# Kernel tuning notes

Hardware: AMD Instinct MI355X
Metric: run time of the kernel (lower is better)

The kernel has to match this reference:

```python
import jax, jax.numpy as jnp
import numpy as np

N_HEADS, D_MODEL, D_KEY = 16, 1024, 64
B, T = 8, 512
SCALE = D_KEY ** (-0.5)


def setup_inputs() -> dict:
    key = jax.random.key(0)
    k1, k2, k3, k4, k5, k6 = jax.random.split(key, 6)
    return {
        "v": jax.random.normal(k1, (B, T, D_MODEL), jnp.float32),
        "mask": jax.random.randint(k2, (B, T, T), 0, 2).astype(bool),
        "w_kqs_w": 0.02 * jax.random.normal(k3, (2 * N_HEADS * D_KEY, D_MODEL), jnp.float32),
        "w_kqs_b": 0.02 * jax.random.normal(k4, (2 * N_HEADS * D_KEY,), jnp.float32),
        "fc_w": 0.02 * jax.random.normal(k5, (D_MODEL, N_HEADS * D_MODEL), jnp.float32),
        "fc_b": 0.02 * jax.random.normal(k6, (D_MODEL,), jnp.float32),
    }


def reference(v, mask, w_kqs_w, w_kqs_b, fc_w, fc_b):
    b, t, d = v.shape
    # kq projection: [b,t,2*H*dk] -> split as (head, 2*dk) per einops 'b t (head k)'
    kq = v @ w_kqs_w.T + w_kqs_b
    kq = kq.reshape(b, t, N_HEADS, 2 * D_KEY).transpose(2, 0, 1, 3)  # [h,b,t,2dk]
    k, q = jnp.split(kq, 2, axis=-1)  # each [h,b,t,dk]
    attn = jnp.einsum('hbqd,hbkd->hbqk', q, k) * SCALE  # [h,b,t,t]
    attn = jnp.where(mask, jnp.float32(-100000.0), attn)  # mask [b,t,t] broadcasts over heads
    attn = jax.nn.softmax(attn, axis=-1)
    # non-projected V broadcast across heads: out [h,b,t,d_model]
    out = jnp.einsum('hbqk,bkc->hbqc', attn, v)
    out = out.transpose(1, 2, 0, 3).reshape(b, t, N_HEADS * d)  # 'head b t c -> b t (head c)'
    out = out @ fc_w.T + fc_b
    return out, attn
```

## Files before the change

kernel.cpp:

```cpp
#include <hip/hip_runtime.h>
#include <cstdint>


typedef __attribute__((ext_vector_type(8))) short short8;
typedef __attribute__((ext_vector_type(4))) float f32x4;

__device__ __forceinline__ unsigned short f2bf(float x) {
  unsigned int u = __float_as_uint(x);
  u += 0x7FFFu + ((u >> 16) & 1u);
  return (unsigned short)(u >> 16);
}

__device__ __forceinline__ void gld16(void* lds, const void* g) {
  __builtin_amdgcn_global_load_lds(
      (const __attribute__((address_space(1))) void*)g,
      (__attribute__((address_space(3))) void*)lds, 16, 0, 0);
}

template<int N> __device__ __forceinline__ void wait_barrier() {
  if constexpr (N == 0)      asm volatile("s_waitcnt vmcnt(0)\n\ts_barrier" ::: "memory");
  else if constexpr (N == 3) asm volatile("s_waitcnt vmcnt(3)\n\ts_barrier" ::: "memory");
  else if constexpr (N == 4) asm volatile("s_waitcnt vmcnt(4)\n\ts_barrier" ::: "memory");
  else static_assert(N < 0, "unsupported vmcnt");
}

template<int BM>
__device__ __forceinline__ void gemm_bt(
    const short* __restrict__ A, int lda,
    const short* __restrict__ B, int ldb,
    int klen, short* __restrict__ ldsA, short* __restrict__ ldsB,
    f32x4 acc[4][4])
{
  constexpr int THREADS = 2 * BM;
  constexpr int NLOADS = (BM == 256) ? 3 : 4;
  constexpr int ABUF = BM * 32;
  constexpr int BBUF = 128 * 32;
  const int tid = (int)threadIdx.x, lane = tid & 63, wave = tid >> 6;
  const int wr = (wave >> 1) * 64, wc = (wave & 1) * 64;
  const int fr = lane & 15, kc = lane >> 4;

  const int ra0 = tid >> 2,             ca0 = ((tid & 3) ^ ((ra0 >> 1) & 3)) << 3;
  const int a1  = tid + THREADS;
  const int ra1 = a1 >> 2,              ca1 = ((a1 & 3) ^ ((ra1 >> 1) & 3)) << 3;
  const short* pa0 = A + ra0 * lda + ca0;
  const short* pa1 = A + ra1 * lda + ca1;
  const int rb0 = tid >> 2,             cb0 = ((tid & 3) ^ ((rb0 >> 1) & 3)) << 3;
  const short* pb0 = B + (rb0 & 127) * ldb + cb0;
  const short* pb1 = nullptr;
  if constexpr (THREADS == 256) {
    const int b1 = tid + 256;
    const int rb1 = b1 >> 2, cb1 = ((b1 & 3) ^ ((rb1 >> 1) & 3)) << 3;
    pb1 = B + rb1 * ldb + cb1;
  }
  const int aw = wave * 512;

  auto stage = [&](int buf, int k0i) {
    const int k0 = k0i << 5;
    short* dA = ldsA + buf * ABUF;
    short* dB = ldsB + buf * BBUF;
    gld16(dA + aw, pa0 + k0);
    gld16(dA + THREADS * 8 + aw, pa1 + k0);
    gld16(dB + aw, pb0 + k0);
    if constexpr (THREADS == 256) gld16(dB + 2048 + aw, pb1 + k0);
  };

  const int nt = klen >> 5;
  stage(0, 0);

  int cur = 0;
  for (int t = 0; t < nt; ++t) {
    int nxt = cur + 1 == 3 ? 0 : cur + 1;
    if (t + 1 < nt) {
      stage(nxt, t + 1);
      wait_barrier<NLOADS>();
    } else {
      wait_barrier<0>();
    }
    const short* bufA = ldsA + cur * ABUF;
    const short* bufB = ldsB + cur * BBUF;
    short8 af[4], bq[4];
#pragma unroll
    for (int m = 0; m < 4; ++m) {
      int row = wr + m * 16 + fr;
      af[m] = *(const short8*)(bufA + row * 32 + ((kc ^ ((row >> 1) & 3)) << 3));
    }
#pragma unroll
    for (int n = 0; n < 4; ++n) {
      int row = wc + n * 16 + fr;
      bq[n] = *(const short8*)(bufB + row * 32 + ((kc ^ ((row >> 1) & 3)) << 3));
    }
    __builtin_amdgcn_s_setprio(1);
#pragma unroll
    for (int m = 0; m < 4; ++m)
#pragma unroll
      for (int n = 0; n < 4; ++n)
        acc[m][n] = __builtin_amdgcn_mfma_f32_16x16x32_bf16(af[m], bq[n], acc[m][n], 0, 0, 0);
    __builtin_amdgcn_s_setprio(0);
    cur = nxt;
  }
}

#define ZERO_ACC(acc)                          \
  _Pragma("unroll") for (int m = 0; m < 4; ++m) \
  _Pragma("unroll") for (int n = 0; n < 4; ++n) \
    acc[m][n] = (f32x4){0.f, 0.f, 0.f, 0.f};

__global__ __launch_bounds__(256, 3) void proj_kernel(
    const short* __restrict__ vb, const short* __restrict__ wb,
    const float* __restrict__ bias, short* __restrict__ kqk, short* __restrict__ kqq)
{
  __shared__ short ldsA[3 * 128 * 32], ldsB[3 * 128 * 32];
  f32x4 acc[4][4];
  ZERO_ACC(acc)
  const short* A = vb + blockIdx.y * 128 * 1024;
  const short* B = wb + blockIdx.x * 128 * 1024;
  gemm_bt<128>(A, 1024, B, 1024, 1024, ldsA, ldsB, acc);

  const int lane = threadIdx.x & 63, wave = threadIdx.x >> 6;
  const int wr = (wave >> 1) * 64, wc = (wave & 1) * 64;
  const int rg = (lane >> 4) * 4, cl = lane & 15;
#pragma unroll
  for (int m = 0; m < 4; ++m)
#pragma unroll
    for (int n = 0; n < 4; ++n)
#pragma unroll
      for (int r = 0; r < 4; ++r) {
        int row = blockIdx.y * 128 + wr + m * 16 + rg + r;
        int col = blockIdx.x * 128 + wc + n * 16 + cl;
        float val = acc[m][n][r] + bias[col];
        int bb = row >> 9, t = row & 511;
        int h = col >> 7, rr = col & 127;
        int base = ((h * 8 + bb) * 512 + t) * 64;
        unsigned short bv = f2bf(val);
        if (rr < 64) kqk[base + rr] = (short)bv;
        else         kqq[base + rr - 64] = (short)bv;
      }
}

__global__ __launch_bounds__(256) void scores_softmax_kernel(
    const short* __restrict__ kqk, const short* __restrict__ kqq,
    const unsigned char* __restrict__ mask8, const int* __restrict__ flags,
    float* __restrict__ attn_f, short* __restrict__ attn_b)
{
  __shared__ short Kl[256 * 64];
  __shared__ short Ql[64 * 64];
  const int tid = threadIdx.x, lane = tid & 63, wave = tid >> 6;
  const int qt = blockIdx.x, hb = blockIdx.y, b = hb & 7;
  const int fr = lane & 15, kc = lane >> 4;
  const short* Qg = kqq + (hb * 512 + qt * 64) * 64;
  const short* Kg = kqk + hb * 512 * 64;

  f32x4 acc[32];
#pragma unroll
  for (int i = 0; i < 32; ++i) acc[i] = (f32x4){0.f, 0.f, 0.f, 0.f};

#pragma unroll
  for (int j = 0; j < 2; ++j) {
    int g = j * 256 + tid;
    int row = g >> 3, c = (g & 7) ^ (row & 7);
    gld16(Ql + (j * 256 + wave * 64) * 8, Qg + row * 64 + c * 8);
  }
  short8 aq[2];
  for (int half = 0; half < 2; ++half) {
#pragma unroll
    for (int j = 0; j < 8; ++j) {
      int g = j * 256 + tid;
      int row = g >> 3, c = (g & 7) ^ (row & 7);
      gld16(Kl + (j * 256 + wave * 64) * 8, Kg + (half * 256 + row) * 64 + c * 8);
    }
    __syncthreads();
    if (half == 0) {
      int qrow = wave * 16 + fr;
#pragma unroll
      for (int s = 0; s < 2; ++s)
        aq[s] = *(const short8*)(Ql + qrow * 64 + (((s * 4 + kc) ^ (qrow & 7)) << 3));
    }
#pragma unroll
    for (int n = 0; n < 16; ++n) {
      int krow = n * 16 + fr;
      short8 b0 = *(const short8*)(Kl + krow * 64 + ((kc ^ (krow & 7)) << 3));
      short8 b1 = *(const short8*)(Kl + krow * 64 + (((4 + kc) ^ (krow & 7)) << 3));
      acc[half * 16 + n] = __builtin_amdgcn_mfma_f32_16x16x32_bf16(aq[0], b0, acc[half * 16 + n], 0, 0, 0);
      acc[half * 16 + n] = __builtin_amdgcn_mfma_f32_16x16x32_bf16(aq[1], b1, acc[half * 16 + n], 0, 0, 0);
    }
    if (half == 0) __syncthreads();
  }

  const int f_byte = flags[0], f_f32 = flags[1];
  const int* mask32 = (const int*)mask8;
  const float* maskf = (const float*)mask8;
  const int qbase = qt * 64 + wave * 16 + (lane >> 4) * 4;

  float mrow[4] = {-3.0e38f, -3.0e38f, -3.0e38f, -3.0e38f};
#pragma unroll
  for (int n = 0; n < 32; ++n) {
    int col = n * 16 + fr;
#pragma unroll
    for (int r = 0; r < 4; ++r) {
      int midx = (b * 512 + qbase + r) * 512 + col;
      bool msk = f_byte ? (mask8[midx] != 0)
                        : (f_f32 ? (maskf[midx] != 0.0f) : (mask32[midx] != 0));
      float s = msk ? -100000.0f : acc[n][r] * 0.125f;
      acc[n][r] = s;
      mrow[r] = fmaxf(mrow[r], s);
    }
  }
#pragma unroll
  for (int r = 0; r < 4; ++r) {
    float v = mrow[r];
    v = fmaxf(v, __shfl_xor(v, 1));
    v = fmaxf(v, __shfl_xor(v, 2));
    v = fmaxf(v, __shfl_xor(v, 4));
    v = fmaxf(v, __shfl_xor(v, 8));
    mrow[r] = v;
  }
  float srow[4] = {0.f, 0.f, 0.f, 0.f};
#pragma unroll
  for (int n = 0; n < 32; ++n)
#pragma unroll
    for (int r = 0; r < 4; ++r) {
      float p = __expf(acc[n][r] - mrow[r]);
      acc[n][r] = p;
      srow[r] += p;
    }
#pragma unroll
  for (int r = 0; r < 4; ++r) {
    float v = srow[r];
    v += __shfl_xor(v, 1);
    v += __shfl_xor(v, 2);
    v += __shfl_xor(v, 4);
    v += __shfl_xor(v, 8);
    srow[r] = 1.0f / v;
  }
  const long obase = (long)hb * 512 * 512;
#pragma unroll
  for (int n = 0; n < 32; ++n) {
    int col = n * 16 + fr;
#pragma unroll
    for (int r = 0; r < 4; ++r) {
      long idx = obase + (long)(qbase + r) * 512 + col;
      float p = acc[n][r] * srow[r];
      attn_f[idx] = p;
      attn_b[idx] = (short)f2bf(p);
    }
  }
}

__global__ __launch_bounds__(512, 4) void pv_kernel(
    const short* __restrict__ attn_b, const short* __restrict__ vT,
    short* __restrict__ out_pre)
{
  __shared__ short ldsA[3 * 256 * 32], ldsB[3 * 128 * 32];
  f32x4 acc[4][4];
  ZERO_ACC(acc)
  const int L = blockIdx.x;
  const int xcd = L & 7, s = L >> 3;
  const int z = xcd + 8 * (s >> 4);
  const int inner = s & 15, x = inner & 7, y = inner >> 3;
  const int h = z >> 3, b = z & 7;
  const short* A = attn_b + ((long)z * 512 + y * 256) * 512;
  const short* B = vT + (b * 1024 + x * 128) * 512;
  gemm_bt<256>(A, 512, B, 512, 512, ldsA, ldsB, acc);

  const int lane = threadIdx.x & 63, wave = threadIdx.x >> 6;
  const int wr = (wave >> 1) * 64, wc = (wave & 1) * 64;
  const int rg = (lane >> 4) * 4, cl = lane & 15;
#pragma unroll
  for (int m = 0; m < 4; ++m)
#pragma unroll
    for (int n = 0; n < 4; ++n)
#pragma unroll
      for (int r = 0; r < 4; ++r) {
        int q = y * 256 + wr + m * 16 + rg + r;
        int c = x * 128 + wc + n * 16 + cl;
        out_pre[((b * 512 + q) * 16 + h) * 1024 + c] = (short)f2bf(acc[m][n][r]);
      }
}

__global__ __launch_bounds__(512, 4) void fc_kernel(
    const short* __restrict__ outp, const short* __restrict__ fcw,
    float* __restrict__ part)
{
  __shared__ short ldsA[3 * 256 * 32], ldsB[3 * 128 * 32];
  f32x4 acc[4][4];
  ZERO_ACC(acc)
  const int L = blockIdx.x;
  const int xcd = L & 7, s = L >> 3;
  const int x = s & 7;
  const int band = xcd * 8 + (s >> 3);
  const int y = band & 15, kz = band >> 4;
  const short* A = outp + (long)y * 256 * 16384 + kz * 4096;
  const short* B = fcw + (long)x * 128 * 16384 + kz * 4096;
  gemm_bt<256>(A, 16384, B, 16384, 4096, ldsA, ldsB, acc);

  float* P = part + (long)kz * 4194304;
  const int lane = threadIdx.x & 63, wave = threadIdx.x >> 6;
  const int wr = (wave >> 1) * 64, wc = (wave & 1) * 64;
  const int rg = (lane >> 4) * 4, cl = lane & 15;
#pragma unroll
  for (int m = 0; m < 4; ++m)
#pragma unroll
    for (int n = 0; n < 4; ++n)
#pragma unroll
      for (int r = 0; r < 4; ++r) {
        int row = y * 256 + wr + m * 16 + rg + r;
        int col = x * 128 + wc + n * 16 + cl;
        P[row * 1024 + col] = acc[m][n][r];
      }
}

__global__ void fc_reduce_kernel(const float* __restrict__ part,
                                 const float* __restrict__ fcb,
                                 float* __restrict__ out)
{
  int i = blockIdx.x * 256 + threadIdx.x;
  f32x4 s = ((const f32x4*)part)[i];
  s += ((const f32x4*)(part + 4194304))[i];
  s += ((const f32x4*)(part + 2 * 4194304))[i];
  s += ((const f32x4*)(part + 3 * 4194304))[i];
  int j = (i * 4) & 1023;
  f32x4 bias = *(const f32x4*)(fcb + j);
  ((f32x4*)out)[i] = s + bias;
}

__global__ void cvt_kernel(const float* __restrict__ in, short* __restrict__ out, int n8) {
  int i = blockIdx.x * 256 + threadIdx.x;
  if (i >= n8) return;
  f32x4 x0 = ((const f32x4*)in)[i * 2];
  f32x4 x1 = ((const f32x4*)in)[i * 2 + 1];
  short8 o;
  o[0] = (short)f2bf(x0[0]); o[1] = (short)f2bf(x0[1]);
  o[2] = (short)f2bf(x0[2]); o[3] = (short)f2bf(x0[3]);
  o[4] = (short)f2bf(x1[0]); o[5] = (short)f2bf(x1[1]);
  o[6] = (short)f2bf(x1[2]); o[7] = (short)f2bf(x1[3]);
  ((short8*)out)[i] = o;
}

__global__ void transpose_kernel(const float* __restrict__ v, short* __restrict__ vT) {
  __shared__ float tile[32][33];
  int b = blockIdx.z, t0 = blockIdx.y * 32, c0 = blockIdx.x * 32;
  int tx = threadIdx.x, ty = threadIdx.y;
  const float* src = v + (b * 512 + t0) * 1024 + c0;
#pragma unroll
  for (int i = 0; i < 4; ++i)
    tile[ty + i * 8][tx] = src[(ty + i * 8) * 1024 + tx];
  __syncthreads();
  short* dst = vT + (b * 1024 + c0) * 512 + t0;
#pragma unroll
  for (int i = 0; i < 4; ++i)
    dst[(ty + i * 8) * 512 + tx] = (short)f2bf(tile[tx][ty + i * 8]);
}

__global__ void detect_kernel(const unsigned int* __restrict__ m, int nwords, int* flags) {
  int i = blockIdx.x * 256 + threadIdx.x;
  unsigned int f0 = 0, f1 = 0;
  for (int idx = i; idx < nwords; idx += gridDim.x * 256) {
    unsigned int u = m[idx];
    f0 |= (u >> 8) & 0xFFu;
    f1 |= u & 0xFFFF0000u;
  }
  int b0 = __any(f0 != 0), b1 = __any(f1 != 0);
  if ((threadIdx.x & 63) == 0) {
    if (b0) atomicOr(flags, 1);
    if (b1) atomicOr(flags + 1, 1);
  }
}

extern "C" void kernel_launch(void* const* d_in, const int* in_sizes, int n_in,
                              void* d_out, int out_size, void* d_ws, size_t ws_size,
                              hipStream_t stream) {
  const float* v   = (const float*)d_in[0];
  const unsigned char* mask = (const unsigned char*)d_in[1];
  const float* wkq = (const float*)d_in[2];
  const float* bkq = (const float*)d_in[3];
  const float* fcw = (const float*)d_in[4];
  const float* fcb = (const float*)d_in[5];
  float* out    = (float*)d_out;
  float* attn_f = out + 4194304;

  char* ws = (char*)d_ws;
  int*   flags = (int*)ws;
  short* vb    = (short*)(ws + 256);
  short* vt    = (short*)(ws + 8388864);
  short* wkqb  = (short*)(ws + 16777472);
  short* fcwb  = (short*)(ws + 20971776);
  short* kqk   = (short*)(ws + 54526208);
  short* kqq   = (short*)(ws + 62914816);
  short* attnb = (short*)(ws + 71303424);
  short* outp  = (short*)(ws + 138412288);
  float* part  = (float*)(ws + 71303424);

  hipMemsetAsync(d_ws, 0, 64, stream);
  detect_kernel<<<256, 256, 0, stream>>>((const unsigned int*)mask, 524288, flags);
  cvt_kernel<<<2048, 256, 0, stream>>>(v, vb, 524288);
  transpose_kernel<<<dim3(32, 16, 8), dim3(32, 8), 0, stream>>>(v, vt);
  cvt_kernel<<<1024, 256, 0, stream>>>(wkq, wkqb, 262144);
  cvt_kernel<<<8192, 256, 0, stream>>>(fcw, fcwb, 2097152);
  proj_kernel<<<dim3(16, 32), 256, 0, stream>>>(vb, wkqb, bkq, kqk, kqq);
  scores_softmax_kernel<<<dim3(8, 128), 256, 0, stream>>>(kqk, kqq, mask, flags, attn_f, attnb);
  pv_kernel<<<2048, 512, 0, stream>>>(attnb, vt, outp);
  fc_kernel<<<512, 512, 0, stream>>>(outp, fcwb, part);
  fc_reduce_kernel<<<4096, 256, 0, stream>>>(part, fcb, out);
}
```

Measured before the change: 663.8 us.

## Pack mask into bitmask and deepen GEMM prefetch to two stages

Adds a kernel that compresses the boolean mask into 64-bit ballot words once, so the scores/softmax kernel loads one small bitmask tile into LDS instead of re-reading the byte mask for every head. The shared GEMM loop now prefetches two K-tiles ahead across its three LDS buffers, with an extra barrier per iteration. The softmax exponent sum is also split into two accumulators. This trades an extra launch and more synchronisation for far less mask traffic across the 16 heads and more latency hiding in the GEMMs.

After: 557.4 us. -16.0%, faster.

```diff
diff --git a/kernel.cpp b/kernel.cpp
--- a/kernel.cpp
+++ b/kernel.cpp
@@ -21,7 +21,12 @@
   if constexpr (N == 0)      asm volatile("s_waitcnt vmcnt(0)\n\ts_barrier" ::: "memory");
   else if constexpr (N == 3) asm volatile("s_waitcnt vmcnt(3)\n\ts_barrier" ::: "memory");
   else if constexpr (N == 4) asm volatile("s_waitcnt vmcnt(4)\n\ts_barrier" ::: "memory");
+  else if constexpr (N == 6) asm volatile("s_waitcnt vmcnt(6)\n\ts_barrier" ::: "memory");
+  else if constexpr (N == 8) asm volatile("s_waitcnt vmcnt(8)\n\ts_barrier" ::: "memory");
   else static_assert(N < 0, "unsupported vmcnt");
+}
+__device__ __forceinline__ void barrier_only() {
+  asm volatile("s_barrier" ::: "memory");
 }
 
 template<int BM>
@@ -66,12 +71,15 @@
 
   const int nt = klen >> 5;
   stage(0, 0);
+  if (nt > 1) stage(1, 1);
 
   int cur = 0;
   for (int t = 0; t < nt; ++t) {
-    int nxt = cur + 1 == 3 ? 0 : cur + 1;
-    if (t + 1 < nt) {
-      stage(nxt, t + 1);
+    if (t + 2 < nt) {
+      int dst = (cur >= 1) ? cur - 1 : cur + 2;
+      stage(dst, t + 2);
+      wait_barrier<2 * NLOADS>();
+    } else if (t + 1 < nt) {
       wait_barrier<NLOADS>();
     } else {
       wait_barrier<0>();
@@ -96,7 +104,8 @@
       for (int n = 0; n < 4; ++n)
         acc[m][n] = __builtin_amdgcn_mfma_f32_16x16x32_bf16(af[m], bq[n], acc[m][n], 0, 0, 0);
     __builtin_amdgcn_s_setprio(0);
-    cur = nxt;
+    barrier_only();
+    cur = (cur >= 2) ? 0 : cur + 1;
   }
 }
 
@@ -139,16 +148,18 @@
 
 __global__ __launch_bounds__(256) void scores_softmax_kernel(
     const short* __restrict__ kqk, const short* __restrict__ kqq,
-    const unsigned char* __restrict__ mask8, const int* __restrict__ flags,
+    const unsigned long long* __restrict__ mbits,
     float* __restrict__ attn_f, short* __restrict__ attn_b)
 {
   __shared__ short Kl[256 * 64];
   __shared__ short Ql[64 * 64];
+  __shared__ unsigned long long Ml[64 * 8];
   const int tid = threadIdx.x, lane = tid & 63, wave = tid >> 6;
   const int qt = blockIdx.x, hb = blockIdx.y, b = hb & 7;
   const int fr = lane & 15, kc = lane >> 4;
   const short* Qg = kqq + (hb * 512 + qt * 64) * 64;
   const short* Kg = kqk + hb * 512 * 64;
+  const unsigned long long* Mg = mbits + ((long)(b * 512) + qt * 64) * 8;
 
   f32x4 acc[32];
 #pragma unroll
@@ -160,6 +171,8 @@
     int row = g >> 3, c = (g & 7) ^ (row & 7);
     gld16(Ql + (j * 256 + wave * 64) * 8, Qg + row * 64 + c * 8);
   }
+  gld16((char*)Ml + wave * 1024, (const char*)Mg + tid * 16);
+
   short8 aq[2];
   for (int half = 0; half < 2; ++half) {
 #pragma unroll
@@ -186,24 +199,26 @@
     if (half == 0) __syncthreads();
   }
 
-  const int f_byte = flags[0], f_f32 = flags[1];
-  const int* mask32 = (const int*)mask8;
-  const float* maskf = (const float*)mask8;
-  const int qbase = qt * 64 + wave * 16 + (lane >> 4) * 4;
-
-  float mrow[4] = {-3.0e38f, -3.0e38f, -3.0e38f, -3.0e38f};
-#pragma unroll
-  for (int n = 0; n < 32; ++n) {
-    int col = n * 16 + fr;
-#pragma unroll
-    for (int r = 0; r < 4; ++r) {
-      int midx = (b * 512 + qbase + r) * 512 + col;
-      bool msk = f_byte ? (mask8[midx] != 0)
-                        : (f_f32 ? (maskf[midx] != 0.0f) : (mask32[midx] != 0));
-      float s = msk ? -100000.0f : acc[n][r] * 0.125f;
-      acc[n][r] = s;
-      mrow[r] = fmaxf(mrow[r], s);
-    }
+  const int lrow0 = wave * 16 + kc * 4;
+  float mrow[4], srow[4];
+#pragma unroll
+  for (int r = 0; r < 4; ++r) {
+    const unsigned long long* mw = Ml + (lrow0 + r) * 8;
+    float mx = -3.0e38f;
+#pragma unroll
+    for (int w = 0; w < 8; ++w) {
+      unsigned long long sh = mw[w] >> fr;
+      unsigned int lo = (unsigned int)sh, hi = (unsigned int)(sh >> 32);
+#pragma unroll
+      for (int nn = 0; nn < 4; ++nn) {
+        int n = w * 4 + nn;
+        unsigned int bit = ((nn < 2 ? lo : hi) >> ((nn & 1) << 4)) & 1u;
+        float s = bit ? -100000.0f : acc[n][r] * 0.125f;
+        acc[n][r] = s;
+        mx = fmaxf(mx, s);
+      }
+    }
+    mrow[r] = mx;
   }
 #pragma unroll
   for (int r = 0; r < 4; ++r) {
@@ -214,15 +229,18 @@
     v = fmaxf(v, __shfl_xor(v, 8));
     mrow[r] = v;
   }
-  float srow[4] = {0.f, 0.f, 0.f, 0.f};
-#pragma unroll
-  for (int n = 0; n < 32; ++n)
-#pragma unroll
-    for (int r = 0; r < 4; ++r) {
-      float p = __expf(acc[n][r] - mrow[r]);
-      acc[n][r] = p;
-      srow[r] += p;
-    }
+#pragma unroll
+  for (int r = 0; r < 4; ++r) {
+    float s0 = 0.f, s1 = 0.f;
+#pragma unroll
+    for (int n = 0; n < 32; n += 2) {
+      float p0 = __expf(acc[n][r] - mrow[r]);
+      float p1 = __expf(acc[n + 1][r] - mrow[r]);
+      acc[n][r] = p0; acc[n + 1][r] = p1;
+      s0 += p0; s1 += p1;
+    }
+    srow[r] = s0 + s1;
+  }
 #pragma unroll
   for (int r = 0; r < 4; ++r) {
     float v = srow[r];
@@ -232,6 +250,7 @@
     v += __shfl_xor(v, 8);
     srow[r] = 1.0f / v;
   }
+  const int qbase = qt * 64 + lrow0;
   const long obase = (long)hb * 512 * 512;
 #pragma unroll
   for (int n = 0; n < 32; ++n) {
@@ -366,6 +385,21 @@
   }
 }
 
+__global__ void maskbits_kernel(const unsigned char* __restrict__ mask8,
+                                const int* __restrict__ flags,
+                                unsigned long long* __restrict__ mbits) {
+  int word = blockIdx.x * 4 + (threadIdx.x >> 6);
+  int lane = threadIdx.x & 63;
+  long e = (long)(word >> 3) * 512 + (word & 7) * 64 + lane;
+  const int f_byte = flags[0], f_f32 = flags[1];
+  bool nz;
+  if (f_byte)      nz = mask8[e] != 0;
+  else if (f_f32)  nz = ((const float*)mask8)[e] != 0.0f;
+  else             nz = ((const int*)mask8)[e] != 0;
+  unsigned long long bl = __ballot(nz);
+  if (lane == 0) mbits[word] = bl;
+}
+
 extern "C" void kernel_launch(void* const* d_in, const int* in_sizes, int n_in,
                               void* d_out, int out_size, void* d_ws, size_t ws_size,
                               hipStream_t stream) {
@@ -380,24 +414,26 @@
 
   char* ws = (char*)d_ws;
   int*   flags = (int*)ws;
-  short* vb    = (short*)(ws + 256);
-  short* vt    = (short*)(ws + 8388864);
-  short* wkqb  = (short*)(ws + 16777472);
-  short* fcwb  = (short*)(ws + 20971776);
-  short* kqk   = (short*)(ws + 54526208);
-  short* kqq   = (short*)(ws + 62914816);
-  short* attnb = (short*)(ws + 71303424);
-  short* outp  = (short*)(ws + 138412288);
-  float* part  = (float*)(ws + 71303424);
+  unsigned long long* mbits = (unsigned long long*)(ws + 4096);
+  short* vb    = (short*)(ws + 270336);
+  short* vt    = (short*)(ws + 8658944);
+  short* wkqb  = (short*)(ws + 17047552);
+  short* fcwb  = (short*)(ws + 21241856);
+  short* kqk   = (short*)(ws + 54796288);
+  short* kqq   = (short*)(ws + 63184896);
+  short* attnb = (short*)(ws + 71573504);
+  short* outp  = (short*)(ws + 138682368);
+  float* part  = (float*)(ws + 71573504);
 
   hipMemsetAsync(d_ws, 0, 64, stream);
   detect_kernel<<<256, 256, 0, stream>>>((const unsigned int*)mask, 524288, flags);
+  maskbits_kernel<<<8192, 256, 0, stream>>>(mask, flags, mbits);
   cvt_kernel<<<2048, 256, 0, stream>>>(v, vb, 524288);
   transpose_kernel<<<dim3(32, 16, 8), dim3(32, 8), 0, stream>>>(v, vt);
   cvt_kernel<<<1024, 256, 0, stream>>>(wkq, wkqb, 262144);
   cvt_kernel<<<8192, 256, 0, stream>>>(fcw, fcwb, 2097152);
   proj_kernel<<<dim3(16, 32), 256, 0, stream>>>(vb, wkqb, bkq, kqk, kqq);
-  scores_softmax_kernel<<<dim3(8, 128), 256, 0, stream>>>(kqk, kqq, mask, flags, attn_f, attnb);
+  scores_softmax_kernel<<<dim3(8, 128), 256, 0, stream>>>(kqk, kqq, mbits, attn_f, attnb);
   pv_kernel<<<2048, 512, 0, stream>>>(attnb, vt, outp);
   fc_kernel<<<512, 512, 0, stream>>>(outp, fcwb, part);
   fc_reduce_kernel<<<4096, 256, 0, stream>>>(part, fcb, out);
```
